# Optimization experiments

Measured on AMD Instinct MI355X. Metric: run time of the kernel, lower is better.

## Reference

```python
import jax, jax.numpy as jnp
import numpy as np

N_NODES = 100000
N_EDGES = 1600000
IN_CH = 128
OUT_CH = 64


def setup_inputs() -> dict:
    key = jax.random.key(0)
    k1, k2, k3 = jax.random.split(key, 3)
    x = jax.random.normal(k1, (N_NODES, IN_CH), dtype=jnp.float32)
    edge_index = jax.random.randint(k2, (2, N_EDGES), 0, N_NODES, dtype=jnp.int32)
    # Glorot-style init for the GCN weight
    W = jax.random.normal(k3, (IN_CH, OUT_CH), dtype=jnp.float32) * (1.0 / np.sqrt(IN_CH))
    b = jnp.zeros((OUT_CH,), dtype=jnp.float32)
    return {"x": x, "edge_index": edge_index, "W": W, "b": b}


def reference(x, edge_index, W, b):
    # GCNConv (PyG semantics): linear transform, add self loops,
    # symmetric deg^{-1/2} normalization, scatter-add aggregation, bias; then ReLU.
    n = x.shape[0]
    h = x @ W  # [N, out]

    loops = jnp.arange(n, dtype=edge_index.dtype)
    row = jnp.concatenate([edge_index[0], loops])  # source nodes
    col = jnp.concatenate([edge_index[1], loops])  # target nodes

    deg = jax.ops.segment_sum(jnp.ones_like(col, dtype=h.dtype), col, num_segments=n)
    deg_inv_sqrt = jnp.where(deg > 0, jax.lax.rsqrt(jnp.maximum(deg, 1e-12)), 0.0)
    norm = deg_inv_sqrt[row] * deg_inv_sqrt[col]  # [E+N]

    msg = h[row] * norm[:, None]  # gather + scale
    out = jax.ops.segment_sum(msg, col, num_segments=n)  # scatter-add
    return jax.nn.relu(out + b)
```

## Files before the change

### kernel.cpp

```cpp
#include <hip/hip_runtime.h>
#include <hip/hip_fp16.h>

#define INC 128
#define OUTC 64
#define MAXBUK 512
#define CAP 6144

typedef __attribute__((ext_vector_type(8))) short short8;
typedef __attribute__((ext_vector_type(4))) float f32x4;

__device__ __forceinline__ ushort f2bf(float f) {
    union { float f; unsigned u; } v; v.f = f;
    unsigned r = v.u + 0x7FFF + ((v.u >> 16) & 1);
    return (ushort)(r >> 16);
}

__global__ __launch_bounds__(512) void buk_fill_kernel(const int* __restrict__ rowi,
                                                       const int* __restrict__ coli,
                                                       int* __restrict__ cursor,
                                                       int* __restrict__ packed,
                                                       int E, int nbuk, int per) {
    __shared__ int lcnt[MAXBUK];
    __shared__ int lbase[MAXBUK];
    int tid = threadIdx.x;
    int c0 = blockIdx.x * per;
    int c1 = min(E, c0 + per);
    for (int t = tid; t < nbuk; t += 512) lcnt[t] = 0;
    __syncthreads();
    for (int e = c0 + tid; e < c1; e += 512)
        atomicAdd(&lcnt[coli[e] >> 8], 1);
    __syncthreads();
    for (int t = tid; t < nbuk; t += 512) {
        int c = lcnt[t];
        if (c) lbase[t] = atomicAdd(&cursor[t], c);
        lcnt[t] = 0;
    }
    __syncthreads();
    for (int e = c0 + tid; e < c1; e += 512) {
        int s = rowi[e], d = coli[e];
        int bk = d >> 8;
        int pos = lbase[bk] + atomicAdd(&lcnt[bk], 1);
        if (pos < CAP)
            packed[(size_t)bk * CAP + pos] = (s << 8) | (d & 255);
    }
}

__global__ __launch_bounds__(1024) void csr_kernel(const int* __restrict__ packed,
                                                   const int* __restrict__ cursor,
                                                   int* __restrict__ csr,
                                                   int* __restrict__ rowptr,
                                                   int* __restrict__ degI,
                                                   float* __restrict__ dinv, int n) {
    __shared__ int cnt[256];
    __shared__ int sc[256];
    __shared__ int cur[256];
    int k = blockIdx.x, tid = threadIdx.x;
    if (tid < 256) cnt[tid] = 0;
    __syncthreads();
    int m = min(cursor[k], CAP);
    const int* pk = packed + (size_t)k * CAP;
    for (int e = tid; e < m; e += 1024)
        atomicAdd(&cnt[pk[e] & 255], 1);
    __syncthreads();
    int c = (tid < 256) ? cnt[tid] : 0;
    if (tid < 256) sc[tid] = c;
    __syncthreads();
    #pragma unroll
    for (int off = 1; off < 256; off <<= 1) {
        int t = (tid >= off && tid < 256) ? sc[tid - off] : 0;
        __syncthreads();
        if (tid < 256) sc[tid] += t;
        __syncthreads();
    }
    if (tid < 256) {
        int ex = sc[tid] - c;
        cur[tid] = ex;
        int node = (k << 8) + tid;
        if (node < n) {
            rowptr[node] = k * CAP + ex;
            degI[node]   = c;
            dinv[node]   = rsqrtf(1.0f + (float)c);
        }
    }
    __syncthreads();
    int* ck = csr + (size_t)k * CAP;
    for (int e = tid; e < m; e += 1024) {
        int p = pk[e];
        int pos = atomicAdd(&cur[p & 255], 1);
        ck[pos] = (int)((((unsigned)p) >> 8) << 7);
    }
}

#define WT_STRIDE 136
__global__ __launch_bounds__(256) void gemm_kernel(
        const float* __restrict__ x, const float* __restrict__ W,
        const float* __restrict__ dinv, __half2* __restrict__ g2, int n) {
    __shared__ ushort WT[OUTC * WT_STRIDE];
    int tid = threadIdx.x;
    #pragma unroll
    for (int i = 0; i < 8; ++i) {
        int idx4 = tid + i * 256;
        float4 v = ((const float4*)W)[idx4];
        int e = idx4 * 4;
        int k = e >> 6, nn = e & 63;
        WT[(nn + 0) * WT_STRIDE + k] = f2bf(v.x);
        WT[(nn + 1) * WT_STRIDE + k] = f2bf(v.y);
        WT[(nn + 2) * WT_STRIDE + k] = f2bf(v.z);
        WT[(nn + 3) * WT_STRIDE + k] = f2bf(v.w);
    }
    __syncthreads();

    int w = tid >> 6, lane = tid & 63;
    int m = lane & 15, quad = lane >> 4;
    int rbase = blockIdx.x * 128 + w * 32;

    short8 afrag[2][4];
    #pragma unroll
    for (int rt = 0; rt < 2; ++rt) {
        int row = rbase + rt * 16 + m;
        #pragma unroll
        for (int kc = 0; kc < 4; ++kc) {
            float4 v0 = make_float4(0.f, 0.f, 0.f, 0.f), v1 = v0;
            if (row < n) {
                const float* p = x + (size_t)row * INC + kc * 32 + quad * 8;
                v0 = *(const float4*)p;
                v1 = *(const float4*)(p + 4);
            }
            short8 a;
            a[0] = (short)f2bf(v0.x); a[1] = (short)f2bf(v0.y);
            a[2] = (short)f2bf(v0.z); a[3] = (short)f2bf(v0.w);
            a[4] = (short)f2bf(v1.x); a[5] = (short)f2bf(v1.y);
            a[6] = (short)f2bf(v1.z); a[7] = (short)f2bf(v1.w);
            afrag[rt][kc] = a;
        }
    }

    f32x4 acc[2][4];
    #pragma unroll
    for (int rt = 0; rt < 2; ++rt)
        #pragma unroll
        for (int nt = 0; nt < 4; ++nt)
            acc[rt][nt] = (f32x4){0.f, 0.f, 0.f, 0.f};

    #pragma unroll
    for (int nt = 0; nt < 4; ++nt) {
        #pragma unroll
        for (int kc = 0; kc < 4; ++kc) {
            short8 bf = *(const short8*)&WT[(nt * 16 + m) * WT_STRIDE + kc * 32 + quad * 8];
            acc[0][nt] = __builtin_amdgcn_mfma_f32_16x16x32_bf16(afrag[0][kc], bf, acc[0][nt], 0, 0, 0);
            acc[1][nt] = __builtin_amdgcn_mfma_f32_16x16x32_bf16(afrag[1][kc], bf, acc[1][nt], 0, 0, 0);
        }
    }

    #pragma unroll
    for (int rt = 0; rt < 2; ++rt) {
        #pragma unroll
        for (int reg = 0; reg < 4; ++reg) {
            int r2 = rbase + rt * 16 + quad * 4 + reg;
            if (r2 < n) {
                float di = dinv[r2];
                #pragma unroll
                for (int nt = 0; nt < 2; ++nt)
                    g2[(size_t)r2 * 32 + nt * 16 + m] =
                        __floats2half2_rn(acc[rt][nt][reg] * di, acc[rt][nt + 2][reg] * di);
            }
        }
    }
}

__global__ __launch_bounds__(256) void agg_kernel(const int* __restrict__ csr,
                                                  const int* __restrict__ rowptr,
                                                  const int* __restrict__ degI,
                                                  const __half2* __restrict__ g2,
                                                  const float* __restrict__ b,
                                                  float* __restrict__ out, int n, int nwav) {
    int w = blockIdx.x * 4 + (threadIdx.x >> 6);
    int lane = threadIdx.x & 63;
    int l = lane & 31, half = lane >> 5;
    const char* gbase = (const char*)g2;
    unsigned lo4 = (unsigned)l * 4u;
    float bx = b[l], by = b[l + 32];
    for (int node = w; node < n; node += nwav) {
        int j = rowptr[node];
        int nd = degI[node];
        int e1 = j + nd;
        float2 s = __half22float2(*(const __half2*)(gbase + (((unsigned)node) << 7) + lo4));
        float ax = 0.f, ay = 0.f;
        for (; j + 16 <= e1; j += 16) {
            unsigned o0 = (unsigned)csr[j + half]      + lo4;
            unsigned o1 = (unsigned)csr[j + 2 + half]  + lo4;
            unsigned o2 = (unsigned)csr[j + 4 + half]  + lo4;
            unsigned o3 = (unsigned)csr[j + 6 + half]  + lo4;
            unsigned o4 = (unsigned)csr[j + 8 + half]  + lo4;
            unsigned o5 = (unsigned)csr[j + 10 + half] + lo4;
            unsigned o6 = (unsigned)csr[j + 12 + half] + lo4;
            unsigned o7 = (unsigned)csr[j + 14 + half] + lo4;
            float2 f0 = __half22float2(*(const __half2*)(gbase + o0));
            float2 f1 = __half22float2(*(const __half2*)(gbase + o1));
            float2 f2 = __half22float2(*(const __half2*)(gbase + o2));
            float2 f3 = __half22float2(*(const __half2*)(gbase + o3));
            float2 f4 = __half22float2(*(const __half2*)(gbase + o4));
            float2 f5 = __half22float2(*(const __half2*)(gbase + o5));
            float2 f6 = __half22float2(*(const __half2*)(gbase + o6));
            float2 f7 = __half22float2(*(const __half2*)(gbase + o7));
            ax += ((f0.x + f1.x) + (f2.x + f3.x)) + ((f4.x + f5.x) + (f6.x + f7.x));
            ay += ((f0.y + f1.y) + (f2.y + f3.y)) + ((f4.y + f5.y) + (f6.y + f7.y));
        }
        if (j + 8 <= e1) {
            unsigned o0 = (unsigned)csr[j + half]     + lo4;
            unsigned o1 = (unsigned)csr[j + 2 + half] + lo4;
            unsigned o2 = (unsigned)csr[j + 4 + half] + lo4;
            unsigned o3 = (unsigned)csr[j + 6 + half] + lo4;
            float2 f0 = __half22float2(*(const __half2*)(gbase + o0));
            float2 f1 = __half22float2(*(const __half2*)(gbase + o1));
            float2 f2 = __half22float2(*(const __half2*)(gbase + o2));
            float2 f3 = __half22float2(*(const __half2*)(gbase + o3));
            ax += (f0.x + f1.x) + (f2.x + f3.x);
            ay += (f0.y + f1.y) + (f2.y + f3.y);
            j += 8;
        }
        for (; j + 2 <= e1; j += 2) {
            unsigned o = (unsigned)csr[j + half] + lo4;
            float2 f = __half22float2(*(const __half2*)(gbase + o));
            ax += f.x; ay += f.y;
        }
        if (j < e1 && half == 0) {
            unsigned o = (unsigned)csr[j] + lo4;
            float2 f = __half22float2(*(const __half2*)(gbase + o));
            ax += f.x; ay += f.y;
        }
        ax += __shfl_xor(ax, 32);
        ay += __shfl_xor(ay, 32);
        if (half == 0) {
            float di = rsqrtf(1.0f + (float)nd);
            out[(size_t)node * OUTC + l]      = fmaxf((ax + s.x) * di + bx, 0.f);
            out[(size_t)node * OUTC + 32 + l] = fmaxf((ay + s.y) * di + by, 0.f);
        }
    }
}

extern "C" void kernel_launch(void* const* d_in, const int* in_sizes, int n_in,
                              void* d_out, int out_size, void* d_ws, size_t ws_size,
                              hipStream_t stream) {
    const float* x  = (const float*)d_in[0];
    const int*   ei = (const int*)d_in[1];
    const float* W  = (const float*)d_in[2];
    const float* b  = (const float*)d_in[3];
    float* out = (float*)d_out;

    int n = in_sizes[0] / INC;
    int E = in_sizes[1] / 2;
    const int* rowi = ei;
    const int* coli = ei + E;

    int nbuk = (n + 255) >> 8;
    int n_pad = ((n + 255) / 256) * 256;

    char* ws = (char*)d_ws;
    int*     cursor = (int*)ws;                  ws += (size_t)MAXBUK * 4;
    float*   dinv   = (float*)ws;                ws += (size_t)n_pad * 4;
    int*     degI   = (int*)ws;                  ws += (size_t)n_pad * 4;
    int*     rowptr = (int*)ws;                  ws += (size_t)n_pad * 4;
    int*     packed = (int*)ws;                  ws += (size_t)nbuk * CAP * 4;
    int*     csr    = (int*)ws;                  ws += (size_t)nbuk * CAP * 4;
    __half2* g2     = (__half2*)ws;

    int fblocks = 512;
    int per = (E + fblocks - 1) / fblocks;

    hipMemsetAsync(cursor, 0, (size_t)MAXBUK * 4, stream);
    buk_fill_kernel<<<fblocks, 512, 0, stream>>>(rowi, coli, cursor, packed, E, nbuk, per);
    csr_kernel<<<nbuk, 1024, 0, stream>>>(packed, cursor, csr, rowptr, degI, dinv, n);
    gemm_kernel<<<(n + 127) / 128, 256, 0, stream>>>(x, W, dinv, g2, n);
    int ablocks = 2048;
    agg_kernel<<<ablocks, 256, 0, stream>>>(csr, rowptr, degI, g2, b, out, n, ablocks * 4);
}
```

Measured before the change: 183.4 us.

## Stage bucket fill in LDS and split aggregation feature slices across blocks

Result: slower. 252.4 us (+37.6%).

```diff
diff --git a/kernel.cpp b/kernel.cpp
--- a/kernel.cpp
+++ b/kernel.cpp
@@ -5,6 +5,7 @@
 #define OUTC 64
 #define MAXBUK 512
 #define CAP 6144
+#define FCH 3200
 
 typedef __attribute__((ext_vector_type(8))) short short8;
 typedef __attribute__((ext_vector_type(4))) float f32x4;
@@ -20,28 +21,49 @@
                                                        int* __restrict__ cursor,
                                                        int* __restrict__ packed,
                                                        int E, int nbuk, int per) {
-    __shared__ int lcnt[MAXBUK];
-    __shared__ int lbase[MAXBUK];
+    __shared__ int lcnt[512];
+    __shared__ int sc[512];
+    __shared__ int lbase[512];
+    __shared__ int sp[FCH];
+    __shared__ ushort sb[FCH];
     int tid = threadIdx.x;
     int c0 = blockIdx.x * per;
     int c1 = min(E, c0 + per);
-    for (int t = tid; t < nbuk; t += 512) lcnt[t] = 0;
+    lcnt[tid] = 0;
     __syncthreads();
     for (int e = c0 + tid; e < c1; e += 512)
         atomicAdd(&lcnt[coli[e] >> 8], 1);
     __syncthreads();
-    for (int t = tid; t < nbuk; t += 512) {
-        int c = lcnt[t];
-        if (c) lbase[t] = atomicAdd(&cursor[t], c);
-        lcnt[t] = 0;
-    }
+    int v = lcnt[tid];
+    sc[tid] = v;
+    __syncthreads();
+    #pragma unroll
+    for (int off = 1; off < 512; off <<= 1) {
+        int t = (tid >= off) ? sc[tid - off] : 0;
+        __syncthreads();
+        sc[tid] += t;
+        __syncthreads();
+    }
+    int ex = sc[tid] - v;
+    int gb = 0;
+    if (v) gb = atomicAdd(&cursor[tid], v);
+    lbase[tid] = gb - ex;
+    lcnt[tid] = ex;
     __syncthreads();
     for (int e = c0 + tid; e < c1; e += 512) {
         int s = rowi[e], d = coli[e];
         int bk = d >> 8;
-        int pos = lbase[bk] + atomicAdd(&lcnt[bk], 1);
-        if (pos < CAP)
-            packed[(size_t)bk * CAP + pos] = (s << 8) | (d & 255);
+        int pos = atomicAdd(&lcnt[bk], 1);
+        sp[pos] = (s << 8) | (d & 255);
+        sb[pos] = (ushort)bk;
+    }
+    __syncthreads();
+    int m = c1 - c0;
+    for (int t = tid; t < m; t += 512) {
+        int bk = sb[t];
+        int p = lbase[bk] + t;
+        if (p < CAP)
+            packed[(size_t)bk * CAP + p] = sp[t];
     }
 }
 
@@ -173,68 +195,50 @@
                                                   const int* __restrict__ degI,
                                                   const __half2* __restrict__ g2,
                                                   const float* __restrict__ b,
-                                                  float* __restrict__ out, int n, int nwav) {
-    int w = blockIdx.x * 4 + (threadIdx.x >> 6);
+                                                  float* __restrict__ out, int n) {
+    int bid = blockIdx.x;
+    int s = (bid & 7) >> 1;
+    int wis = ((bid >> 3) * 2 + (bid & 1)) * 4 + (threadIdx.x >> 6);
     int lane = threadIdx.x & 63;
-    int l = lane & 31, half = lane >> 5;
+    int g = lane >> 3, c2 = lane & 7;
     const char* gbase = (const char*)g2;
-    unsigned lo4 = (unsigned)l * 4u;
-    float bx = b[l], by = b[l + 32];
-    for (int node = w; node < n; node += nwav) {
+    unsigned so = (unsigned)(s * 32 + c2 * 4);
+    int ch = ((lane & 8) ? 32 : 0) + s * 8 + c2;
+    float bb = b[ch];
+    for (int node = wis; node < n; node += 2048) {
         int j = rowptr[node];
         int nd = degI[node];
         int e1 = j + nd;
-        float2 s = __half22float2(*(const __half2*)(gbase + (((unsigned)node) << 7) + lo4));
         float ax = 0.f, ay = 0.f;
         for (; j + 16 <= e1; j += 16) {
-            unsigned o0 = (unsigned)csr[j + half]      + lo4;
-            unsigned o1 = (unsigned)csr[j + 2 + half]  + lo4;
-            unsigned o2 = (unsigned)csr[j + 4 + half]  + lo4;
-            unsigned o3 = (unsigned)csr[j + 6 + half]  + lo4;
-            unsigned o4 = (unsigned)csr[j + 8 + half]  + lo4;
-            unsigned o5 = (unsigned)csr[j + 10 + half] + lo4;
-            unsigned o6 = (unsigned)csr[j + 12 + half] + lo4;
-            unsigned o7 = (unsigned)csr[j + 14 + half] + lo4;
+            unsigned o0 = (unsigned)csr[j + g] + so;
+            unsigned o1 = (unsigned)csr[j + 8 + g] + so;
             float2 f0 = __half22float2(*(const __half2*)(gbase + o0));
             float2 f1 = __half22float2(*(const __half2*)(gbase + o1));
-            float2 f2 = __half22float2(*(const __half2*)(gbase + o2));
-            float2 f3 = __half22float2(*(const __half2*)(gbase + o3));
-            float2 f4 = __half22float2(*(const __half2*)(gbase + o4));
-            float2 f5 = __half22float2(*(const __half2*)(gbase + o5));
-            float2 f6 = __half22float2(*(const __half2*)(gbase + o6));
-            float2 f7 = __half22float2(*(const __half2*)(gbase + o7));
-            ax += ((f0.x + f1.x) + (f2.x + f3.x)) + ((f4.x + f5.x) + (f6.x + f7.x));
-            ay += ((f0.y + f1.y) + (f2.y + f3.y)) + ((f4.y + f5.y) + (f6.y + f7.y));
+            ax += f0.x + f1.x;
+            ay += f0.y + f1.y;
         }
         if (j + 8 <= e1) {
-            unsigned o0 = (unsigned)csr[j + half]     + lo4;
-            unsigned o1 = (unsigned)csr[j + 2 + half] + lo4;
-            unsigned o2 = (unsigned)csr[j + 4 + half] + lo4;
-            unsigned o3 = (unsigned)csr[j + 6 + half] + lo4;
+            unsigned o0 = (unsigned)csr[j + g] + so;
             float2 f0 = __half22float2(*(const __half2*)(gbase + o0));
-            float2 f1 = __half22float2(*(const __half2*)(gbase + o1));
-            float2 f2 = __half22float2(*(const __half2*)(gbase + o2));
-            float2 f3 = __half22float2(*(const __half2*)(gbase + o3));
-            ax += (f0.x + f1.x) + (f2.x + f3.x);
-            ay += (f0.y + f1.y) + (f2.y + f3.y);
+            ax += f0.x; ay += f0.y;
             j += 8;
         }
-        for (; j + 2 <= e1; j += 2) {
-            unsigned o = (unsigned)csr[j + half] + lo4;
+        int r = e1 - j;
+        if (g < r) {
+            unsigned o = (unsigned)csr[j + g] + so;
             float2 f = __half22float2(*(const __half2*)(gbase + o));
             ax += f.x; ay += f.y;
         }
-        if (j < e1 && half == 0) {
-            unsigned o = (unsigned)csr[j] + lo4;
-            float2 f = __half22float2(*(const __half2*)(gbase + o));
-            ax += f.x; ay += f.y;
-        }
-        ax += __shfl_xor(ax, 32);
-        ay += __shfl_xor(ay, 32);
-        if (half == 0) {
+        ax += __shfl_xor(ax, 8);  ax += __shfl_xor(ax, 16);  ax += __shfl_xor(ax, 32);
+        ay += __shfl_xor(ay, 8);  ay += __shfl_xor(ay, 16);  ay += __shfl_xor(ay, 32);
+        if (lane < 16) {
+            unsigned os = (((unsigned)node) << 7) + (unsigned)(s * 32 + c2 * 4);
+            float2 fs = __half22float2(*(const __half2*)(gbase + os));
             float di = rsqrtf(1.0f + (float)nd);
-            out[(size_t)node * OUTC + l]      = fmaxf((ax + s.x) * di + bx, 0.f);
-            out[(size_t)node * OUTC + 32 + l] = fmaxf((ay + s.y) * di + by, 0.f);
+            float tot  = (lane & 8) ? ay   : ax;
+            float self = (lane & 8) ? fs.y : fs.x;
+            out[(size_t)node * OUTC + ch] = fmaxf((tot + self) * di + bb, 0.f);
         }
     }
 }
@@ -272,6 +276,5 @@
     buk_fill_kernel<<<fblocks, 512, 0, stream>>>(rowi, coli, cursor, packed, E, nbuk, per);
     csr_kernel<<<nbuk, 1024, 0, stream>>>(packed, cursor, csr, rowptr, degI, dinv, n);
     gemm_kernel<<<(n + 127) / 128, 256, 0, stream>>>(x, W, dinv, g2, n);
-    int ablocks = 2048;
-    agg_kernel<<<ablocks, 256, 0, stream>>>(csr, rowptr, degI, g2, b, out, n, ablocks * 4);
-}
+    agg_kernel<<<2048, 256, 0, stream>>>(csr, rowptr, degI, g2, b, out, n);
+}
```
